# Performance work log

Hardware: AMD Instinct MI355X
Metric: run time of the kernel (lower is better)

## Reference

```python
import jax, jax.numpy as jnp
import numpy as np

B, N, C, H = 8, 1025, 512, 8
G = 32  # grid size; S = G*G = N-1


def setup_inputs() -> dict:
    key = jax.random.key(0)
    ks = jax.random.split(key, 5)
    return {
        "x": jax.random.normal(ks[0], (B, N, C), dtype=jnp.float32),
        "qkv_w": jax.random.normal(ks[1], (3 * C, C), dtype=jnp.float32) * (C ** -0.5),
        "proj_w": jax.random.normal(ks[2], (C, C), dtype=jnp.float32) * (C ** -0.5),
        "proj_b": jnp.zeros((C,), dtype=jnp.float32),
        "wg_w": jax.random.normal(ks[3], (H, 64), dtype=jnp.float32) * 0.125,
        "wg_b": jnp.zeros((H,), dtype=jnp.float32),
    }


def _geometry_bias(wg_w, wg_b):
    # BoxRelationalEmbedding on a fixed 32x32 grid; batch-independent, so computed once.
    S = G * G
    xs = jnp.arange(G, dtype=jnp.float32)
    px = jnp.repeat(xs, G)   # px_min: row index per flattened cell
    py = jnp.tile(xs, G)     # py_min: col index per flattened cell
    rx0, ry0 = px / G, py / G
    rx1, ry1 = (px + 1.0) / G, (py + 1.0) / G
    cx = 0.5 * (rx0 + rx1)
    cy = 0.5 * (ry0 + ry1)
    w = rx1 - rx0 + 1.0
    h = ry1 - ry0 + 1.0
    dx = jnp.log(jnp.clip(jnp.abs((cx[:, None] - cx[None, :]) / w[:, None]), 1e-3, None))
    dy = jnp.log(jnp.clip(jnp.abs((cy[:, None] - cy[None, :]) / h[:, None]), 1e-3, None))
    dw = jnp.log(w[:, None] / w[None, :])
    dh = jnp.log(h[:, None] / h[None, :])
    pos = jnp.stack([dx, dy, dw, dh], axis=-1)  # [S,S,4]
    dim_mat = 1.0 / jnp.power(1000.0, jnp.arange(8, dtype=jnp.float32) / 8.0)  # dim_g/8 = 8 freqs
    mul = (100.0 * pos)[..., None] * dim_mat        # [S,S,4,8]
    mul = mul.reshape(S, S, 32)
    emb = jnp.concatenate([jnp.sin(mul), jnp.cos(mul)], axis=-1)  # [S,S,64]
    rgw = jax.nn.relu(jnp.einsum('ijd,hd->hij', emb, wg_w) + wg_b[:, None, None])  # [H,S,S]
    rgw = jnp.log(jnp.clip(rgw, 1e-6, None))
    # pad zero column (dim 3 cat of t1) then zero row (dim 2 cat of t2) -> [H, S+1, S+1]
    return jnp.pad(rgw, ((0, 0), (1, 0), (1, 0)))


def reference(x, qkv_w, proj_w, proj_b, wg_w, wg_b):
    b, n, c = x.shape
    hd = c // H
    scale = hd ** -0.5
    bias = _geometry_bias(wg_w, wg_b)  # [H, n, n]
    qkv = (x @ qkv_w.T).reshape(b, n, 3, H, hd)
    q, k, v = qkv[:, :, 0], qkv[:, :, 1], qkv[:, :, 2]  # each [b,n,H,hd]
    attn = jnp.einsum('bihd,bjhd->bhij', q, k) * scale + bias[None]
    attn = jax.nn.softmax(attn, axis=-1)
    out = jnp.einsum('bhij,bjhd->bihd', attn, v).reshape(b, n, c)
    return out @ proj_w.T + proj_b
```

## Files before the change

kernel.cpp:

```cpp
#include <hip/hip_runtime.h>
#include <hip/hip_bf16.h>
#include <hip/hip_fp16.h>
#include <math.h>

#define B_  8
#define N_  1025
#define C_  512
#define H_  8
#define HD_ 64
#define M_  (B_ * N_)
#define VCS 2560
#define VST 36
#define BW_ 1056
#define PER_ ((size_t)B_ * H_ * N_ * HD_)
#define EXP_BLKS 256
#define GK 512

typedef __attribute__((ext_vector_type(8))) short short8;
typedef __attribute__((ext_vector_type(4))) float f32x4;
typedef __attribute__((ext_vector_type(4))) unsigned short us4;

__device__ inline unsigned short bf16u(float x) {
    __hip_bfloat16 t = __float2bfloat16(x);
    return *(unsigned short*)&t;
}
__device__ inline float fexp2(float x) {
    float r;
    asm("v_exp_f32 %0, %1" : "=v"(r) : "v"(x));
    return r;
}
__device__ inline float h2f(unsigned short u) {
    __half_raw hr; hr.x = u;
    return __half2float(__half(hr));
}
__device__ inline void load_lds16(const void* g, void* l) {
    __builtin_amdgcn_global_load_lds(
        (const __attribute__((address_space(1))) unsigned int*)g,
        (__attribute__((address_space(3))) unsigned int*)l, 16, 0, 0);
}
__device__ inline short8 pack8(float4 u0, float4 u1) {
    short8 r;
    r[0] = (short)bf16u(u0.x); r[1] = (short)bf16u(u0.y);
    r[2] = (short)bf16u(u0.z); r[3] = (short)bf16u(u0.w);
    r[4] = (short)bf16u(u1.x); r[5] = (short)bf16u(u1.y);
    r[6] = (short)bf16u(u1.z); r[7] = (short)bf16u(u1.w);
    return r;
}

struct TileRegs { float4 a0, a1, a2, a3, b0, b1, b2, b3; };

__global__ __launch_bounds__(256) void gemm_qkv_mfma(
        const float* __restrict__ x, const float* __restrict__ qkv_w,
        const float* __restrict__ wg_w, const float* __restrict__ wg_b,
        unsigned short* __restrict__ qb, unsigned short* __restrict__ kb,
        unsigned short* __restrict__ vtc, unsigned short* __restrict__ big) {
    __shared__ __align__(16) unsigned short As[2][4096];
    __shared__ __align__(16) unsigned short Bs[2][4096];
    int lin = blockIdx.x;
    int tid = threadIdx.x;

    if (lin < EXP_BLKS) {
        float* tl = (float*)&As[0][0];
        float* sT = (float*)&Bs[0][0];
        float* cT = sT + 256;
        int h = lin >> 5, rs = lin & 31;
        const float* w = wg_w + h * 64;
        {
            const float fr[8] = {1.0f, 0.421696503f, 0.177827941f, 0.074989421f,
                                 0.031622777f, 0.013335214f, 0.005623413f, 0.002371374f};
            int a = tid >> 3, k = tid & 7;
            float dxv = logf(fmaxf((float)a * (1.0f / 33.0f), 0.001f));
            float ang = 100.0f * dxv * fr[k];
            sT[tid] = sinf(ang);
            cT[tid] = cosf(ang);
        }
        __syncthreads();
        float wb = wg_b[h];
        float wtail = 0.f;
#pragma unroll
        for (int k = 0; k < 8; k++) wtail += w[48 + k] + w[56 + k];
#pragma unroll 1
        for (int e = tid; e < 1024; e += 256) {
            int a = e >> 5, b = e & 31;
            float acc = wb + wtail;
#pragma unroll
            for (int k = 0; k < 8; k++) {
                acc += w[k]      * sT[a * 8 + k];
                acc += w[8 + k]  * sT[b * 8 + k];
                acc += w[32 + k] * cT[a * 8 + k];
                acc += w[40 + k] * cT[b * 8 + k];
            }
            tl[e] = log2f(fmaxf(fmaxf(acc, 0.0f), 1e-6f));
        }
        __syncthreads();
        int rbase = rs * 36;
#pragma unroll 1
        for (int e8 = tid; e8 < 36 * 132; e8 += 256) {
            int rr = e8 / 132;
            int cg = e8 - rr * 132;
            int r = rbase + rr;
            int c0 = cg * 8;
            int i = min(r, 1024) - 1;
            int ix = i >> 5, iy = i & 31;
            unsigned short o8[8];
#pragma unroll
            for (int e = 0; e < 8; e++) {
                int c = c0 + e;
                float v;
                if (r == 0 || c == 0) v = 0.f;
                else if (c > 1024)    v = -60000.f;
                else {
                    int j = c - 1;
                    int da = __sad(ix, j >> 5, 0u);
                    int db = __sad(iy, j & 31, 0u);
                    v = tl[da * 32 + db];
                }
                __half hv = __float2half(v);
                o8[e] = *(unsigned short*)&hv;
            }
            *(short8*)(big + ((size_t)h * 1152 + r) * BW_ + c0) = *(short8*)o8;
        }
        return;
    }

    int orig = lin - EXP_BLKS;
    int xcd = orig & 7, pos = orig >> 3;
    int wgid = (xcd < 4) ? xcd * 98 + pos : 392 + (xcd - 4) * 97 + pos;
    int bx = wgid % 12, by = wgid / 12;

    int wv = tid >> 6, lane = tid & 63;
    int quad = lane >> 4, l16 = lane & 15;
    int m0 = by * 128, n0 = bx * 128;
    int wr = (wv >> 1) * 64, wc = (wv & 1) * 64;

    int ar0 = min(m0 + (tid >> 2), M_ - 1);
    int ar1 = min(m0 + 64 + (tid >> 2), M_ - 1);
    int br0 = n0 + (tid >> 2), br1 = n0 + 64 + (tid >> 2);
    int ac = (tid & 3) * 8;

    int which = n0 >> 9;
    int h = ((n0 + wc) >> 6) & 7;

    f32x4 acc[4][4];
    const f32x4 zero4 = {0.f, 0.f, 0.f, 0.f};
#pragma unroll
    for (int mi = 0; mi < 4; mi++)
#pragma unroll
        for (int ni = 0; ni < 4; ni++) acc[mi][ni] = zero4;

    auto loadT = [&](int t, TileRegs& r) {
        int k0 = t * 32;
        const float* pa0 = x + (size_t)ar0 * GK + k0 + ac;
        const float* pa1 = x + (size_t)ar1 * GK + k0 + ac;
        const float* pb0 = qkv_w + (size_t)br0 * GK + k0 + ac;
        const float* pb1 = qkv_w + (size_t)br1 * GK + k0 + ac;
        r.a0 = *(const float4*)pa0; r.a1 = *(const float4*)(pa0 + 4);
        r.a2 = *(const float4*)pa1; r.a3 = *(const float4*)(pa1 + 4);
        r.b0 = *(const float4*)pb0; r.b1 = *(const float4*)(pb0 + 4);
        r.b2 = *(const float4*)pb1; r.b3 = *(const float4*)(pb1 + 4);
    };
    int wrow = tid >> 2;
    int wg = ((tid & 3) ^ (wrow >> 1)) & 3;
    auto writeT = [&](const TileRegs& r, int buf) {
        *(short8*)&As[buf][wrow * 32 + wg * 8]        = pack8(r.a0, r.a1);
        *(short8*)&As[buf][(wrow + 64) * 32 + wg * 8] = pack8(r.a2, r.a3);
        *(short8*)&Bs[buf][wrow * 32 + wg * 8]        = pack8(r.b0, r.b1);
        *(short8*)&Bs[buf][(wrow + 64) * 32 + wg * 8] = pack8(r.b2, r.b3);
    };
    auto compute = [&](int buf) {
        short8 af[4], bf[4];
#pragma unroll
        for (int mi = 0; mi < 4; mi++) {
            int rr = wr + mi * 16 + l16;
            af[mi] = *(const short8*)&As[buf][rr * 32 + ((quad ^ (rr >> 1)) & 3) * 8];
        }
#pragma unroll
        for (int ni = 0; ni < 4; ni++) {
            int rr = wc + ni * 16 + l16;
            bf[ni] = *(const short8*)&Bs[buf][rr * 32 + ((quad ^ (rr >> 1)) & 3) * 8];
        }
#pragma unroll
        for (int mi = 0; mi < 4; mi++)
#pragma unroll
            for (int ni = 0; ni < 4; ni++)
                acc[mi][ni] = __builtin_amdgcn_mfma_f32_16x16x32_bf16(
                    bf[ni], af[mi], acc[mi][ni], 0, 0, 0);
    };

    TileRegs tA, tB;
    loadT(0, tA);
    writeT(tA, 0);
    loadT(1, tB);

#pragma unroll 1
    for (int kk = 0; kk < 16; kk += 2) {
        __syncthreads();
        if (kk + 2 < 16) loadT(kk + 2, tA);
        compute(0);
        if (kk + 1 < 16) writeT(tB, 1);
        __syncthreads();
        if (kk + 3 < 16) loadT(kk + 3, tB);
        compute(1);
        if (kk + 2 < 16) writeT(tA, 0);
    }

    if (which < 2) {
        unsigned short* dst = (which == 0) ? qb : kb;
        float sc = (which == 0) ? 0.18033688f : 1.0f;
#pragma unroll
        for (int mi = 0; mi < 4; mi++) {
            int m = m0 + wr + mi * 16 + l16;
            if (m < M_) {
                int bb = m / N_;
                int i  = m - bb * N_;
                unsigned short* row = dst + ((size_t)(bb * H_ + h) * N_ + i) * HD_;
#pragma unroll
                for (int ni = 0; ni < 4; ni++) {
                    ushort4 pk;
                    pk.x = bf16u(acc[mi][ni][0] * sc);
                    pk.y = bf16u(acc[mi][ni][1] * sc);
                    pk.z = bf16u(acc[mi][ni][2] * sc);
                    pk.w = bf16u(acc[mi][ni][3] * sc);
                    *(ushort4*)(row + ni * 16 + quad * 4) = pk;
                }
            }
        }
    } else {
#pragma unroll
        for (int mi = 0; mi < 4; mi++) {
            int m = m0 + wr + mi * 16 + l16;
            if (m < M_) {
                int bb = m / N_;
                int i  = m - bb * N_;
                int ch = i >> 5, key = i & 31;
                int slot = ((key >> 2) & 3) * 8 + ((key >> 4) << 2) + (key & 3);
                unsigned short* base = vtc + ((size_t)(bb * H_ + h) * VST + ch) * VCS + slot;
#pragma unroll
                for (int ni = 0; ni < 4; ni++)
#pragma unroll
                    for (int reg = 0; reg < 4; reg++)
                        base[(ni * 16 + quad * 4 + reg) * 40] = bf16u(acc[mi][ni][reg]);
            }
        }
    }
}

struct WRegs { float4 w0, w1; };

__global__ __launch_bounds__(256) void gemm_proj_mfma(
        const unsigned short* __restrict__ A, const float* __restrict__ Wf,
        const float* __restrict__ bias, float* __restrict__ out) {
    __shared__ __align__(16) unsigned short As[2][4096];
    __shared__ __align__(16) unsigned short Bs[2][2048];
    int tid = threadIdx.x;
    int w = tid >> 6, lane = tid & 63;
    int quad = lane >> 4, l16 = lane & 15;

    int orig = blockIdx.x;
    int wgid = (orig & 7) * 65 + (orig >> 3);
    int bn = wgid & 7, bm = wgid >> 3;

    int m0 = bm * 128;
    int n0 = bn * 64;
    int wr = (w >> 1) * 64, wc = (w & 1) * 32;

    int ar0 = min(m0 + (tid >> 2), M_ - 1);
    int ar1 = min(m0 + 64 + (tid >> 2), M_ - 1);
    int brW = n0 + (tid >> 2);
    int acW = (tid & 3) * 8;
    int acA = (((tid & 3) ^ ((tid >> 3) & 3))) * 8;

    f32x4 acc[4][2];
    const f32x4 zero4 = {0.f, 0.f, 0.f, 0.f};
#pragma unroll
    for (int mi = 0; mi < 4; mi++)
#pragma unroll
        for (int ni = 0; ni < 2; ni++) acc[mi][ni] = zero4;

    auto stageA = [&](int t, int buf) {
        int k0 = t * 32;
        load_lds16(A + (size_t)ar0 * GK + k0 + acA, &As[buf][w * 512]);
        load_lds16(A + (size_t)ar1 * GK + k0 + acA, &As[buf][2048 + w * 512]);
    };
    auto loadW = [&](int t, WRegs& r) {
        int k0 = t * 32;
        const float* p0 = Wf + (size_t)brW * GK + k0 + acW;
        r.w0 = *(const float4*)p0; r.w1 = *(const float4*)(p0 + 4);
    };
    int wrow = tid >> 2;
    int wg = ((tid & 3) ^ (wrow >> 1)) & 3;
    auto writeW = [&](const WRegs& r, int buf) {
        *(short8*)&Bs[buf][wrow * 32 + wg * 8] = pack8(r.w0, r.w1);
    };
    auto compute = [&](int buf) {
        short8 af[4], bf[2];
#pragma unroll
        for (int mi = 0; mi < 4; mi++) {
            int rr = wr + mi * 16 + l16;
            af[mi] = *(const short8*)&As[buf][rr * 32 + ((quad ^ (rr >> 1)) & 3) * 8];
        }
#pragma unroll
        for (int ni = 0; ni < 2; ni++) {
            int rr = wc + ni * 16 + l16;
            bf[ni] = *(const short8*)&Bs[buf][rr * 32 + ((quad ^ (rr >> 1)) & 3) * 8];
        }
#pragma unroll
        for (int mi = 0; mi < 4; mi++)
#pragma unroll
            for (int ni = 0; ni < 2; ni++)
                acc[mi][ni] = __builtin_amdgcn_mfma_f32_16x16x32_bf16(
                    af[mi], bf[ni], acc[mi][ni], 0, 0, 0);
    };

    WRegs tA, tB;
    stageA(0, 0);
    loadW(0, tA);
    writeW(tA, 0);
    loadW(1, tB);

#pragma unroll 1
    for (int kk = 0; kk < 16; kk += 2) {
        __syncthreads();
        if (kk + 1 < 16) stageA(kk + 1, 1);
        if (kk + 2 < 16) loadW(kk + 2, tA);
        compute(0);
        if (kk + 1 < 16) writeW(tB, 1);
        __syncthreads();
        if (kk + 2 < 16) stageA(kk + 2, 0);
        if (kk + 3 < 16) loadW(kk + 3, tB);
        compute(1);
        if (kk + 2 < 16) writeW(tA, 0);
    }

    float bvals[2];
#pragma unroll
    for (int ni = 0; ni < 2; ni++) bvals[ni] = bias[n0 + wc + ni * 16 + l16];
#pragma unroll
    for (int mi = 0; mi < 4; mi++)
#pragma unroll
        for (int reg = 0; reg < 4; reg++) {
            int m = m0 + wr + mi * 16 + quad * 4 + reg;
            if (m < M_) {
                float* row = out + (size_t)m * C_ + n0 + wc;
#pragma unroll
                for (int ni = 0; ni < 2; ni++)
                    row[ni * 16 + l16] = acc[mi][ni][reg] + bvals[ni];
            }
        }
}

#define RT_ 288

__global__ __launch_bounds__(576, 3) void attn_fused(
        const unsigned short* __restrict__ qg,
        const unsigned short* __restrict__ kg,
        const unsigned short* __restrict__ vtc,
        const unsigned short* __restrict__ bigtab,
        unsigned short* __restrict__ ob) {
    __shared__ __align__(16) unsigned short Ks[2][6144];
    __shared__ __align__(16) unsigned short Vs[2][7680];

    int tid = threadIdx.x;
    int w = tid >> 6, lane = tid & 63;
    int quad = lane >> 4, l16 = lane & 15;

    int lin = blockIdx.x;
    int bh = lin & 63;
    int mt = lin >> 6;
    int b = bh >> 3, h = bh & 7;

    const unsigned short* qp = qg + (size_t)bh * N_ * HD_;
    const unsigned short* kp = kg + (size_t)bh * N_ * HD_;
    const unsigned short* vp = vtc + (size_t)bh * VST * VCS;

    int qrA = mt * RT_ + w * 32 + l16;
    const unsigned short* btA = bigtab + ((size_t)h * 1152 + qrA) * BW_ + quad * 4;
    const unsigned short* btB = btA + (size_t)16 * BW_;

    short8 qfA[2], qfB[2];
    {
        int rowA = min(qrA, N_ - 1);
        int rowB = min(qrA + 16, N_ - 1);
        qfA[0] = *(const short8*)(qp + (size_t)rowA * HD_ + quad * 8);
        qfA[1] = *(const short8*)(qp + (size_t)rowA * HD_ + 32 + quad * 8);
        qfB[0] = *(const short8*)(qp + (size_t)rowB * HD_ + quad * 8);
        qfB[1] = *(const short8*)(qp + (size_t)rowB * HD_ + 32 + quad * 8);
    }

    f32x4 oA[4], oB[4], lA, lB;
    const f32x4 zero4 = {0.f, 0.f, 0.f, 0.f};
#pragma unroll
    for (int g2 = 0; g2 < 4; g2++) { oA[g2] = zero4; oB[g2] = zero4; }
    lA = zero4; lB = zero4;
    short8 ones;
    {
        short one_bf = (short)0x3F80;
#pragma unroll
        for (int j = 0; j < 8; j++) ones[j] = one_bf;
    }

    auto stage = [&](int t, int buf) {
#pragma unroll
        for (int r2 = 0; r2 < 3; r2++) {
            int cb = w * 3 + r2;
            if (cb < 12) {
                int ch = cb * 64 + lane;
                int ct = ch >> 7, rem = ch & 127;
                int oct = rem >> 4, k16 = rem & 15;
                int key = min(t * 96 + ct * 16 + k16, N_ - 1);
                load_lds16(kp + (size_t)key * HD_ + oct * 8, &Ks[buf][cb * 512]);
            } else {
                int vb = cb - 12;
                load_lds16(vp + (size_t)t * 3 * VCS + (size_t)(vb * 64 + lane) * 8,
                           &Vs[buf][vb * 512]);
            }
        }
    };

    us4 bAc[6], bAn[6];
#pragma unroll
    for (int i = 0; i < 6; i++)
        bAn[i] = *(const us4*)(btA + (i >> 1) * 32 + (i & 1) * 16);
    stage(0, 0);

#pragma unroll 1
    for (int t = 0; t < 11; t++) {
        int buf = t & 1;
        __syncthreads();

#pragma unroll
        for (int i = 0; i < 6; i++) bAc[i] = bAn[i];
        us4 bB[6];
        {
            const unsigned short* btp = btB + t * 96;
#pragma unroll
            for (int i = 0; i < 6; i++)
                bB[i] = *(const us4*)(btp + (i >> 1) * 32 + (i & 1) * 16);
        }
        if (t < 10) {
            const unsigned short* btp = btA + (t + 1) * 96;
#pragma unroll
            for (int i = 0; i < 6; i++)
                bAn[i] = *(const us4*)(btp + (i >> 1) * 32 + (i & 1) * 16);
            stage(t + 1, buf ^ 1);
        }

#pragma unroll
        for (int ks = 0; ks < 3; ks++) {
            f32x4 sA[2], sB[2];
#pragma unroll
            for (int ctl = 0; ctl < 2; ctl++) {
                int ct = ks * 2 + ctl;
                short8 kf0 = *(const short8*)&Ks[buf][(ct * 128 + quad * 16 + l16) * 8];
                short8 kf1 = *(const short8*)&Ks[buf][(ct * 128 + (4 + quad) * 16 + l16) * 8];
                sA[ctl] = __builtin_amdgcn_mfma_f32_16x16x32_bf16(kf0, qfA[0], zero4, 0, 0, 0);
                sA[ctl] = __builtin_amdgcn_mfma_f32_16x16x32_bf16(kf1, qfA[1], sA[ctl], 0, 0, 0);
                sB[ctl] = __builtin_amdgcn_mfma_f32_16x16x32_bf16(kf0, qfB[0], zero4, 0, 0, 0);
                sB[ctl] = __builtin_amdgcn_mfma_f32_16x16x32_bf16(kf1, qfB[1], sB[ctl], 0, 0, 0);
            }
            const unsigned short* vcp = &Vs[buf][ks * 2560 + quad * 8];
            short8 vf[4];
#pragma unroll
            for (int g2 = 0; g2 < 4; g2++)
                vf[g2] = *(const short8*)(vcp + (g2 * 16 + l16) * 40);

            short8 pfA;
#pragma unroll
            for (int e = 0; e < 8; e++) {
                int par = e >> 2, r = e & 3;
                float bia = h2f(bAc[ks * 2 + par][r]);
                pfA[e] = (short)bf16u(fexp2(sA[par][r] + bia));
            }
            __builtin_amdgcn_s_setprio(1);
#pragma unroll
            for (int g2 = 0; g2 < 4; g2++)
                oA[g2] = __builtin_amdgcn_mfma_f32_16x16x32_bf16(pfA, vf[g2], oA[g2], 0, 0, 0);
            lA = __builtin_amdgcn_mfma_f32_16x16x32_bf16(pfA, ones, lA, 0, 0, 0);
            __builtin_amdgcn_s_setprio(0);

            short8 pfB;
#pragma unroll
            for (int e = 0; e < 8; e++) {
                int par = e >> 2, r = e & 3;
                float bia = h2f(bB[ks * 2 + par][r]);
                pfB[e] = (short)bf16u(fexp2(sB[par][r] + bia));
            }
            __builtin_amdgcn_s_setprio(1);
#pragma unroll
            for (int g2 = 0; g2 < 4; g2++)
                oB[g2] = __builtin_amdgcn_mfma_f32_16x16x32_bf16(pfB, vf[g2], oB[g2], 0, 0, 0);
            lB = __builtin_amdgcn_mfma_f32_16x16x32_bf16(pfB, ones, lB, 0, 0, 0);
            __builtin_amdgcn_s_setprio(0);
        }
    }

#pragma unroll
    for (int grp = 0; grp < 2; grp++) {
        int rbase = mt * RT_ + w * 32 + grp * 16 + quad * 4;
        const f32x4* oX = grp ? oB : oA;
        const f32x4& lX = grp ? lB : lA;
#pragma unroll
        for (int reg = 0; reg < 4; reg++) {
            int r = rbase + reg;
            if (r < N_) {
                float inv = 1.0f / lX[reg];
                unsigned short* orow = ob + ((size_t)b * N_ + r) * C_ + h * HD_ + l16;
#pragma unroll
                for (int g2 = 0; g2 < 4; g2++)
                    orow[g2 * 16] = bf16u(oX[g2][reg] * inv);
            }
        }
    }
}

extern "C" void kernel_launch(void* const* d_in, const int* in_sizes, int n_in,
                              void* d_out, int out_size, void* d_ws, size_t ws_size,
                              hipStream_t stream) {
    const float* x      = (const float*)d_in[0];
    const float* qkv_w  = (const float*)d_in[1];
    const float* proj_w = (const float*)d_in[2];
    const float* proj_b = (const float*)d_in[3];
    const float* wg_w   = (const float*)d_in[4];
    const float* wg_b   = (const float*)d_in[5];
    float* out = (float*)d_out;

    const size_t per = PER_;
    char* ws = (char*)d_ws;
    unsigned short* bigtab = (unsigned short*)ws;
    unsigned short* qb     = bigtab + (size_t)8 * 1152 * BW_;
    unsigned short* kb     = qb + per;
    unsigned short* vtc    = kb + per;
    unsigned short* ob     = vtc + (size_t)64 * VST * VCS;

    gemm_qkv_mfma<<<EXP_BLKS + 12 * 65, 256, 0, stream>>>(
        x, qkv_w, wg_w, wg_b, qb, kb, vtc, bigtab);
    attn_fused<<<256, 576, 0, stream>>>(qb, kb, vtc, bigtab, ob);
    gemm_proj_mfma<<<520, 256, 0, stream>>>(ob, proj_w, proj_b, out);
}
```

Measured before the change: 174.7 us.

## Reorder QKV grid blocks, use register-staged A loads in proj GEMM, lighter barriers

The fused QKV kernel now places the GEMM blocks first and the geometry-bias expansion blocks last in the grid, so the heavier GEMM tiles are dispatched earlier. The projection GEMM drops direct global-to-LDS loads for the A operand and instead loads A into registers alongside W, then writes both into swizzled LDS after compute, giving register double-buffering for both operands. Both GEMM loops replace __syncthreads with an inline-asm lgkmcnt wait plus s_barrier, which avoids waiting on outstanding global loads at each barrier. This costs extra VGPRs for A staging and relies on manual waitcnt correctness.

Result: slower. 179.1 us (+2.5%).

```diff
diff --git a/kernel.cpp b/kernel.cpp
--- a/kernel.cpp
+++ b/kernel.cpp
@@ -14,11 +14,14 @@
 #define BW_ 1056
 #define PER_ ((size_t)B_ * H_ * N_ * HD_)
 #define EXP_BLKS 256
+#define GEMM_BLKS 780
 #define GK 512
 
 typedef __attribute__((ext_vector_type(8))) short short8;
 typedef __attribute__((ext_vector_type(4))) float f32x4;
 typedef __attribute__((ext_vector_type(4))) unsigned short us4;
+
+#define BAR_LGKM() asm volatile("s_waitcnt lgkmcnt(0)\n\ts_barrier" ::: "memory")
 
 __device__ inline unsigned short bf16u(float x) {
     __hip_bfloat16 t = __float2bfloat16(x);
@@ -59,11 +62,12 @@
     int lin = blockIdx.x;
     int tid = threadIdx.x;
 
-    if (lin < EXP_BLKS) {
+    if (lin >= GEMM_BLKS) {
+        int elin = lin - GEMM_BLKS;
         float* tl = (float*)&As[0][0];
         float* sT = (float*)&Bs[0][0];
         float* cT = sT + 256;
-        int h = lin >> 5, rs = lin & 31;
+        int h = elin >> 5, rs = elin & 31;
         const float* w = wg_w + h * 64;
         {
             const float fr[8] = {1.0f, 0.421696503f, 0.177827941f, 0.074989421f,
@@ -123,8 +127,7 @@
         return;
     }
 
-    int orig = lin - EXP_BLKS;
-    int xcd = orig & 7, pos = orig >> 3;
+    int xcd = lin & 7, pos = lin >> 3;
     int wgid = (xcd < 4) ? xcd * 98 + pos : 392 + (xcd - 4) * 97 + pos;
     int bx = wgid % 12, by = wgid / 12;
 
@@ -194,11 +197,11 @@
 
 #pragma unroll 1
     for (int kk = 0; kk < 16; kk += 2) {
-        __syncthreads();
+        BAR_LGKM();
         if (kk + 2 < 16) loadT(kk + 2, tA);
         compute(0);
         if (kk + 1 < 16) writeT(tB, 1);
-        __syncthreads();
+        BAR_LGKM();
         if (kk + 3 < 16) loadT(kk + 3, tB);
         compute(1);
         if (kk + 2 < 16) writeT(tA, 0);
@@ -245,7 +248,7 @@
     }
 }
 
-struct WRegs { float4 w0, w1; };
+struct PRegs { short8 a0, a1; float4 w0, w1; };
 
 __global__ __launch_bounds__(256) void gemm_proj_mfma(
         const unsigned short* __restrict__ A, const float* __restrict__ Wf,
@@ -267,8 +270,7 @@
     int ar0 = min(m0 + (tid >> 2), M_ - 1);
     int ar1 = min(m0 + 64 + (tid >> 2), M_ - 1);
     int brW = n0 + (tid >> 2);
-    int acW = (tid & 3) * 8;
-    int acA = (((tid & 3) ^ ((tid >> 3) & 3))) * 8;
+    int ac = (tid & 3) * 8;
 
     f32x4 acc[4][2];
     const f32x4 zero4 = {0.f, 0.f, 0.f, 0.f};
@@ -277,20 +279,19 @@
 #pragma unroll
         for (int ni = 0; ni < 2; ni++) acc[mi][ni] = zero4;
 
-    auto stageA = [&](int t, int buf) {
+    auto loadP = [&](int t, PRegs& r) {
         int k0 = t * 32;
-        load_lds16(A + (size_t)ar0 * GK + k0 + acA, &As[buf][w * 512]);
-        load_lds16(A + (size_t)ar1 * GK + k0 + acA, &As[buf][2048 + w * 512]);
-    };
-    auto loadW = [&](int t, WRegs& r) {
-        int k0 = t * 32;
-        const float* p0 = Wf + (size_t)brW * GK + k0 + acW;
+        r.a0 = *(const short8*)(A + (size_t)ar0 * GK + k0 + ac);
+        r.a1 = *(const short8*)(A + (size_t)ar1 * GK + k0 + ac);
+        const float* p0 = Wf + (size_t)brW * GK + k0 + ac;
         r.w0 = *(const float4*)p0; r.w1 = *(const float4*)(p0 + 4);
     };
     int wrow = tid >> 2;
     int wg = ((tid & 3) ^ (wrow >> 1)) & 3;
-    auto writeW = [&](const WRegs& r, int buf) {
-        *(short8*)&Bs[buf][wrow * 32 + wg * 8] = pack8(r.w0, r.w1);
+    auto writeP = [&](const PRegs& r, int buf) {
+        *(short8*)&As[buf][wrow * 32 + wg * 8]        = r.a0;
+        *(short8*)&As[buf][(wrow + 64) * 32 + wg * 8] = r.a1;
+        *(short8*)&Bs[buf][wrow * 32 + wg * 8]        = pack8(r.w0, r.w1);
     };
     auto compute = [&](int buf) {
         short8 af[4], bf[2];
@@ -312,24 +313,21 @@
                     af[mi], bf[ni], acc[mi][ni], 0, 0, 0);
     };
 
-    WRegs tA, tB;
-    stageA(0, 0);
-    loadW(0, tA);
-    writeW(tA, 0);
-    loadW(1, tB);
+    PRegs tA, tB;
+    loadP(0, tA);
+    writeP(tA, 0);
+    loadP(1, tB);
 
 #pragma unroll 1
     for (int kk = 0; kk < 16; kk += 2) {
-        __syncthreads();
-        if (kk + 1 < 16) stageA(kk + 1, 1);
-        if (kk + 2 < 16) loadW(kk + 2, tA);
+        BAR_LGKM();
+        if (kk + 2 < 16) loadP(kk + 2, tA);
         compute(0);
-        if (kk + 1 < 16) writeW(tB, 1);
-        __syncthreads();
-        if (kk + 2 < 16) stageA(kk + 2, 0);
-        if (kk + 3 < 16) loadW(kk + 3, tB);
+        if (kk + 1 < 16) writeP(tB, 1);
+        BAR_LGKM();
+        if (kk + 3 < 16) loadP(kk + 3, tB);
         compute(1);
-        if (kk + 2 < 16) writeW(tA, 0);
+        if (kk + 2 < 16) writeP(tA, 0);
     }
 
     float bvals[2];
@@ -532,7 +530,7 @@
     unsigned short* vtc    = kb + per;
     unsigned short* ob     = vtc + (size_t)64 * VST * VCS;
 
-    gemm_qkv_mfma<<<EXP_BLKS + 12 * 65, 256, 0, stream>>>(
+    gemm_qkv_mfma<<<GEMM_BLKS + EXP_BLKS, 256, 0, stream>>>(
         x, qkv_w, wg_w, wg_b, qb, kb, vtc, bigtab);
     attn_fused<<<256, 576, 0, stream>>>(qb, kb, vtc, bigtab, ob);
     gemm_proj_mfma<<<520, 256, 0, stream>>>(ob, proj_w, proj_b, out);
```

## Split attention into 128-row tiles with a dedicated wave for the leftover row

Applied to the files above, without the earlier changes.

The attention kernel is re-tiled from 288-row tiles of 9 waves (256 blocks) to 128-row tiles of 4 waves (512 blocks). Since 8×128 = 1024, the last query row (1024) is handled by wave 3 of the last tile through an extra C fragment path. This removes the padded-row work and the bounds checks on output stores. In exchange it adds a divergent branch in that one wave and more staging work per wave, since each now loads 7 chunks instead of 3.

Result: no change. 176.5 us (+1.0%).

```diff
diff --git a/kernel.cpp b/kernel.cpp
--- a/kernel.cpp
+++ b/kernel.cpp
@@ -349,9 +349,9 @@
         }
 }
 
-#define RT_ 288
-
-__global__ __launch_bounds__(576, 3) void attn_fused(
+#define RT_ 128
+
+__global__ __launch_bounds__(256, 2) void attn_fused(
         const unsigned short* __restrict__ qg,
         const unsigned short* __restrict__ kg,
         const unsigned short* __restrict__ vtc,
@@ -368,6 +368,7 @@
     int bh = lin & 63;
     int mt = lin >> 6;
     int b = bh >> 3, h = bh & 7;
+    bool hasC = (mt == 7) && (w == 3);
 
     const unsigned short* qp = qg + (size_t)bh * N_ * HD_;
     const unsigned short* kp = kg + (size_t)bh * N_ * HD_;
@@ -376,22 +377,25 @@
     int qrA = mt * RT_ + w * 32 + l16;
     const unsigned short* btA = bigtab + ((size_t)h * 1152 + qrA) * BW_ + quad * 4;
     const unsigned short* btB = btA + (size_t)16 * BW_;
-
-    short8 qfA[2], qfB[2];
+    const unsigned short* btC = bigtab + ((size_t)h * 1152 + 1024) * BW_ + quad * 4;
+
+    short8 qfA[2], qfB[2], qfC[2];
     {
-        int rowA = min(qrA, N_ - 1);
-        int rowB = min(qrA + 16, N_ - 1);
+        int rowA = qrA;
+        int rowB = qrA + 16;
         qfA[0] = *(const short8*)(qp + (size_t)rowA * HD_ + quad * 8);
         qfA[1] = *(const short8*)(qp + (size_t)rowA * HD_ + 32 + quad * 8);
         qfB[0] = *(const short8*)(qp + (size_t)rowB * HD_ + quad * 8);
         qfB[1] = *(const short8*)(qp + (size_t)rowB * HD_ + 32 + quad * 8);
-    }
-
-    f32x4 oA[4], oB[4], lA, lB;
+        qfC[0] = *(const short8*)(qp + (size_t)(N_ - 1) * HD_ + quad * 8);
+        qfC[1] = *(const short8*)(qp + (size_t)(N_ - 1) * HD_ + 32 + quad * 8);
+    }
+
+    f32x4 oA[4], oB[4], oC[4], lA, lB, lC;
     const f32x4 zero4 = {0.f, 0.f, 0.f, 0.f};
 #pragma unroll
-    for (int g2 = 0; g2 < 4; g2++) { oA[g2] = zero4; oB[g2] = zero4; }
-    lA = zero4; lB = zero4;
+    for (int g2 = 0; g2 < 4; g2++) { oA[g2] = zero4; oB[g2] = zero4; oC[g2] = zero4; }
+    lA = zero4; lB = zero4; lC = zero4;
     short8 ones;
     {
         short one_bf = (short)0x3F80;
@@ -401,15 +405,15 @@
 
     auto stage = [&](int t, int buf) {
 #pragma unroll
-        for (int r2 = 0; r2 < 3; r2++) {
-            int cb = w * 3 + r2;
+        for (int r2 = 0; r2 < 7; r2++) {
+            int cb = w * 7 + r2;
             if (cb < 12) {
                 int ch = cb * 64 + lane;
                 int ct = ch >> 7, rem = ch & 127;
                 int oct = rem >> 4, k16 = rem & 15;
                 int key = min(t * 96 + ct * 16 + k16, N_ - 1);
                 load_lds16(kp + (size_t)key * HD_ + oct * 8, &Ks[buf][cb * 512]);
-            } else {
+            } else if (cb < 27) {
                 int vb = cb - 12;
                 load_lds16(vp + (size_t)t * 3 * VCS + (size_t)(vb * 64 + lane) * 8,
                            &Vs[buf][vb * 512]);
@@ -430,12 +434,18 @@
 
 #pragma unroll
         for (int i = 0; i < 6; i++) bAc[i] = bAn[i];
-        us4 bB[6];
+        us4 bB[6], bC[6];
         {
             const unsigned short* btp = btB + t * 96;
 #pragma unroll
             for (int i = 0; i < 6; i++)
                 bB[i] = *(const us4*)(btp + (i >> 1) * 32 + (i & 1) * 16);
+        }
+        if (hasC) {
+            const unsigned short* btp = btC + t * 96;
+#pragma unroll
+            for (int i = 0; i < 6; i++)
+                bC[i] = *(const us4*)(btp + (i >> 1) * 32 + (i & 1) * 16);
         }
         if (t < 10) {
             const unsigned short* btp = btA + (t + 1) * 96;
@@ -447,7 +457,7 @@
 
 #pragma unroll
         for (int ks = 0; ks < 3; ks++) {
-            f32x4 sA[2], sB[2];
+            f32x4 sA[2], sB[2], sC[2];
 #pragma unroll
             for (int ctl = 0; ctl < 2; ctl++) {
                 int ct = ks * 2 + ctl;
@@ -457,6 +467,10 @@
                 sA[ctl] = __builtin_amdgcn_mfma_f32_16x16x32_bf16(kf1, qfA[1], sA[ctl], 0, 0, 0);
                 sB[ctl] = __builtin_amdgcn_mfma_f32_16x16x32_bf16(kf0, qfB[0], zero4, 0, 0, 0);
                 sB[ctl] = __builtin_amdgcn_mfma_f32_16x16x32_bf16(kf1, qfB[1], sB[ctl], 0, 0, 0);
+                if (hasC) {
+                    sC[ctl] = __builtin_amdgcn_mfma_f32_16x16x32_bf16(kf0, qfC[0], zero4, 0, 0, 0);
+                    sC[ctl] = __builtin_amdgcn_mfma_f32_16x16x32_bf16(kf1, qfC[1], sC[ctl], 0, 0, 0);
+                }
             }
             const unsigned short* vcp = &Vs[buf][ks * 2560 + quad * 8];
             short8 vf[4];
@@ -491,6 +505,20 @@
                 oB[g2] = __builtin_amdgcn_mfma_f32_16x16x32_bf16(pfB, vf[g2], oB[g2], 0, 0, 0);
             lB = __builtin_amdgcn_mfma_f32_16x16x32_bf16(pfB, ones, lB, 0, 0, 0);
             __builtin_amdgcn_s_setprio(0);
+
+            if (hasC) {
+                short8 pfC;
+#pragma unroll
+                for (int e = 0; e < 8; e++) {
+                    int par = e >> 2, r = e & 3;
+                    float bia = h2f(bC[ks * 2 + par][r]);
+                    pfC[e] = (short)bf16u(fexp2(sC[par][r] + bia));
+                }
+#pragma unroll
+                for (int g2 = 0; g2 < 4; g2++)
+                    oC[g2] = __builtin_amdgcn_mfma_f32_16x16x32_bf16(pfC, vf[g2], oC[g2], 0, 0, 0);
+                lC = __builtin_amdgcn_mfma_f32_16x16x32_bf16(pfC, ones, lC, 0, 0, 0);
+            }
         }
     }
 
@@ -502,14 +530,19 @@
 #pragma unroll
         for (int reg = 0; reg < 4; reg++) {
             int r = rbase + reg;
-            if (r < N_) {
-                float inv = 1.0f / lX[reg];
-                unsigned short* orow = ob + ((size_t)b * N_ + r) * C_ + h * HD_ + l16;
-#pragma unroll
-                for (int g2 = 0; g2 < 4; g2++)
-                    orow[g2 * 16] = bf16u(oX[g2][reg] * inv);
-            }
-        }
+            float inv = 1.0f / lX[reg];
+            unsigned short* orow = ob + ((size_t)b * N_ + r) * C_ + h * HD_ + l16;
+#pragma unroll
+            for (int g2 = 0; g2 < 4; g2++)
+                orow[g2 * 16] = bf16u(oX[g2][reg] * inv);
+        }
+    }
+    if (hasC && quad == 0) {
+        float inv = 1.0f / lC[0];
+        unsigned short* orow = ob + ((size_t)b * N_ + 1024) * C_ + h * HD_ + l16;
+#pragma unroll
+        for (int g2 = 0; g2 < 4; g2++)
+            orow[g2 * 16] = bf16u(oC[g2][0] * inv);
     }
 }
 
@@ -532,8 +565,8 @@
     unsigned short* vtc    = kb + per;
     unsigned short* ob     = vtc + (size_t)64 * VST * VCS;
 
-    gemm_qkv_mfma<<<EXP_BLKS + 12 * 65, 256, 0, stream>>>(
+    gemm_qkv_mfma<<<EXP_BLKS + 780, 256, 0, stream>>>(
         x, qkv_w, wg_w, wg_b, qb, kb, vtc, bigtab);
-    attn_fused<<<256, 576, 0, stream>>>(qb, kb, vtc, bigtab, ob);
+    attn_fused<<<512, 256, 0, stream>>>(qb, kb, vtc, bigtab, ob);
     gemm_proj_mfma<<<520, 256, 0, stream>>>(ob, proj_w, proj_b, out);
 }
```
